# Kernel tuning notes

Hardware: AMD Instinct MI355X
Metric: run time of the kernel (lower is better)

Reference implementation:

```python
import jax, jax.numpy as jnp
import numpy as np

B, N, C, H, W = 4, 64, 256, 64, 64
ROI = 7          # roi_samples
S = 3            # ceil(16px / 7) sample points per ROI cell (boxes fixed at 16px)
HALF = 0.125     # fixed normalized half-size -> 16px boxes on 64-grid -> static S
N_INT = ROI * S  # interpolation grid side length (21)


def setup_inputs() -> dict:
    key = jax.random.key(0)
    k1, k2, k3, k4, k5 = jax.random.split(key, 5)
    img = jax.random.normal(k1, (B, C, H, W), jnp.float32)
    cen = jax.random.uniform(k2, (B, N, 2), jnp.float32, minval=0.2, maxval=0.8)
    # boxes_bn22 = [(x1,y1),(x2,y2)], normalized coords, fixed size so that
    # custom_roi_align's ceil(box_px/roi) == S for every box
    boxes = jnp.stack([cen - HALF, cen + HALF], axis=2)  # (B,N,2,2)
    conv_w = jax.random.normal(k3, (C, C, ROI, ROI), jnp.float32) * 0.02
    conv_b = jnp.zeros((C,), jnp.float32)
    cxcywh_w = jax.random.normal(k4, (C, 4), jnp.float32) * 0.02
    cxcywh_b = jnp.zeros((C,), jnp.float32)
    posenc_w = jax.random.normal(k5, (C, C + 2), jnp.float32) * 0.02
    posenc_b = jnp.zeros((C,), jnp.float32)
    return {"image_tokens_bchw": img, "boxes_bn22": boxes,
            "conv_w": conv_w, "conv_b": conv_b,
            "cxcywh_w": cxcywh_w, "cxcywh_b": cxcywh_b,
            "posenc_w": posenc_w, "posenc_b": posenc_b}


def _pe_1d(coord, num_feats):
    # DETR/SAM-style sinusoidal PE of a scalar coordinate -> (n, num_feats)
    dim_t = 10000.0 ** (2.0 * (jnp.arange(num_feats) // 2) / num_feats)
    pos = coord[:, None] * (2.0 * jnp.pi) / dim_t.astype(coord.dtype)
    enc = jnp.stack([jnp.sin(pos[:, 0::2]), jnp.cos(pos[:, 1::2])], axis=-1)
    return enc.reshape(coord.shape[0], num_feats)


def _roi_align(img_bchw, boxes_f4, bidx):
    # Faithful vectorization of custom_roi_align: per-box uniform sample grid,
    # bilinear grid_sample (align_corners=True, border pad), then SxS avg-pool.
    nsx = W / (W - 1.0)
    nsy = H / (H - 1.0)
    t = jnp.arange(N_INT, dtype=img_bchw.dtype) / (N_INT - 1)

    def one(b, box):
        x1, y1, x2, y2 = box[0] * nsx, box[1] * nsy, box[2] * nsx, box[3] * nsy
        hsx = (x2 - x1) / (2 * N_INT)
        hsy = (y2 - y1) / (2 * N_INT)
        gx = (x1 + hsx) + t * (x2 - x1 - 2 * hsx)  # linspace over box interior
        gy = (y1 + hsy) + t * (y2 - y1 - 2 * hsy)
        # align_corners=True pixel coords; border padding == clamp
        px = jnp.clip(gx * (W - 1), 0.0, W - 1.0)
        py = jnp.clip(gy * (H - 1), 0.0, H - 1.0)
        x0f, y0f = jnp.floor(px), jnp.floor(py)
        wx, wy = px - x0f, py - y0f
        x0 = jnp.clip(x0f.astype(jnp.int32), 0, W - 1)
        x1i = jnp.clip(x0 + 1, 0, W - 1)
        y0 = jnp.clip(y0f.astype(jnp.int32), 0, H - 1)
        y1i = jnp.clip(y0 + 1, 0, H - 1)
        img = img_bchw[b]                               # (C,H,W)
        v00 = img[:, y0[:, None], x0[None, :]]          # (C,N_INT,N_INT)
        v01 = img[:, y0[:, None], x1i[None, :]]
        v10 = img[:, y1i[:, None], x0[None, :]]
        v11 = img[:, y1i[:, None], x1i[None, :]]
        top = v00 + (v01 - v00) * wx[None, None, :]
        bot = v10 + (v11 - v10) * wx[None, None, :]
        samp = top + (bot - top) * wy[None, :, None]    # (C,N_INT,N_INT)
        # avg_pool2d with kernel (S,S) stride (S,S)
        return samp.reshape(C, ROI, S, ROI, S).mean(axis=(2, 4))  # (C,ROI,ROI)

    return jax.vmap(one)(bidx, boxes_f4)


def reference(image_tokens_bchw, boxes_bn22, conv_w, conv_b,
              cxcywh_w, cxcywh_b, posenc_w, posenc_b):
    boxes_f4 = boxes_bn22.reshape(B * N, 4)
    bidx = jnp.repeat(jnp.arange(B), N)
    roi = _roi_align(image_tokens_bchw, boxes_f4, bidx)      # (BN,C,ROI,ROI)
    # 7x7 conv over a 7x7 map -> 1x1: a plain contraction
    img_enc = (jnp.einsum('nchw,ochw->no', roi, conv_w) + conv_b).reshape(B, N, C)

    cen = boxes_bn22.mean(axis=2)                            # (B,N,2) cx,cy
    wh = boxes_bn22[:, :, 1] - boxes_bn22[:, :, 0]           # (B,N,2) w,h
    cxcywh = jnp.concatenate([cen, wh], axis=-1)             # (B,N,4)
    flat = cxcywh.reshape(B * N, 4)
    x_enc = _pe_1d(flat[:, 0], C // 2)
    y_enc = _pe_1d(flat[:, 1], C // 2)
    pe_tok = jnp.concatenate([y_enc, x_enc, flat[:, 3:4], flat[:, 2:3]], axis=-1)
    pos_enc = (pe_tok @ posenc_w.T + posenc_b).reshape(B, N, C)
    base = cxcywh @ cxcywh_w.T + cxcywh_b                    # (B,N,C)
    return base + pos_enc + img_enc
```

## Files before the change

### kernel.cpp

```cpp
#include <hip/hip_runtime.h>

static constexpr int KDIM = 12544;
static constexpr float TWO_PI = 6.28318530717958647692f;

typedef float f32x4 __attribute__((ext_vector_type(4)));
typedef short bf16x8 __attribute__((ext_vector_type(8)));

__device__ inline float bf2f(unsigned short u) {
    union { unsigned int i; float f; } x; x.i = ((unsigned int)u) << 16; return x.f;
}
__device__ inline unsigned short f2bf(float f) {
    union { float f; unsigned int i; } x; x.f = f;
    unsigned int r = (x.i + 0x7FFFu + ((x.i >> 16) & 1u)) >> 16;
    return (unsigned short)r;
}

__global__ __launch_bounds__(256) void k_prep(
    const float* __restrict__ boxes,
    const float* __restrict__ cxw, const float* __restrict__ cxb,
    const float* __restrict__ pw,  const float* __restrict__ pb,
    const float* __restrict__ cb,
    const float* __restrict__ img, const float* __restrict__ convw,
    float* __restrict__ out,
    unsigned short* __restrict__ imgT, unsigned short* __restrict__ Wt,
    float4* __restrict__ lutx, float4* __restrict__ luty)
{
    __shared__ float smem[12544];
    const int bid = blockIdx.x;
    const int tid = threadIdx.x;

    if (bid < 256) {
        const int n = bid;
        const float bx1 = boxes[n*4+0], by1 = boxes[n*4+1];
        const float bx2 = boxes[n*4+2], by2 = boxes[n*4+3];
        const float cx = 0.5f*(bx1+bx2), cy = 0.5f*(by1+by2);
        const float wx = bx2-bx1,        wy = by2-by1;

        float* pe = smem;

        if (tid < 128) {
            const int   k     = tid & 63;
            const float coord = (tid < 64) ? cy : cx;
            const float d   = exp2f((float)k * (13.287712379549449f / 64.0f));
            const float arg = coord * TWO_PI / d;
            float s, c;
            sincosf(arg, &s, &c);
            const int base = (tid < 64) ? 0 : 128;
            pe[base + 2*k]     = s;
            pe[base + 2*k + 1] = c;
        } else if (tid == 128) {
            pe[256] = wy;
            pe[257] = wx;
        } else if (tid >= 160 && tid < 202) {
            const int  t   = tid - 160;
            const bool isx = (t < 21);
            const int  i   = isx ? t : (t - 21);
            const float ns = 64.0f / 63.0f;
            const float a1 = (isx ? bx1 : by1) * ns;
            const float a2 = (isx ? bx2 : by2) * ns;
            const float hs = (a2 - a1) * (1.0f / 42.0f);
            const float tt = (float)i * (1.0f / 20.0f);
            const float g  = a1 + hs + tt * (a2 - a1 - 2.0f*hs);
            float p = g * 63.0f;
            p = fminf(fmaxf(p, 0.0f), 63.0f);
            const float p0 = floorf(p);
            const float w  = p - p0;
            int i0 = (int)p0; i0 = min(i0, 63);
            const int i1 = min(i0 + 1, 63);
            (isx ? lutx : luty)[n*21 + i] = make_float4((float)i0, (float)i1, w, 0.0f);
        }
        __syncthreads();

        const int o = tid;
        float acc = pb[o] + cb[o] + cxb[o];
        acc = fmaf(cxw[o*4+0], cx, acc);
        acc = fmaf(cxw[o*4+1], cy, acc);
        acc = fmaf(cxw[o*4+2], wx, acc);
        acc = fmaf(cxw[o*4+3], wy, acc);
        const float* __restrict__ pwr = pw + o*258;
        for (int k = 0; k < 258; ++k)
            acc = fmaf(pe[k], pwr[k], acc);
        out[n*256 + o] = acc;
    } else if (bid < 1280) {
        float (*t)[65] = (float(*)[65])smem;
        const int idx = bid - 256;
        const int b   = idx >> 8;
        const int rem = idx & 255;
        const int c0  = (rem & 3) * 64;
        const int p0  = (rem >> 2) * 64;
        const int col = tid & 63;
        const int r4  = tid >> 6;
        #pragma unroll
        for (int i = 0; i < 16; ++i) {
            const int row = i*4 + r4;
            t[row][col] = img[((size_t)(b*256 + c0 + row)) * 4096 + p0 + col];
        }
        __syncthreads();
        #pragma unroll
        for (int i = 0; i < 16; ++i) {
            const int prow = i*4 + r4;
            imgT[((size_t)(b*4096 + p0 + prow)) * 256 + c0 + col] = f2bf(t[col][prow]);
        }
    } else {
        const int o = bid - 1280;
        #pragma unroll
        for (int i = 0; i < 49; ++i)
            smem[i*256 + tid] = convw[(size_t)o*12544 + i*256 + tid];
        __syncthreads();
        for (int ij = 0; ij < 49; ++ij)
            Wt[(size_t)o*12544 + ij*256 + tid] = f2bf(smem[tid*49 + ij]);
    }
}

__global__ __launch_bounds__(256) void k_fused(
    const unsigned short* __restrict__ imgT,
    const unsigned short* __restrict__ Wt,
    const float4* __restrict__ lutx, const float4* __restrict__ luty,
    float* __restrict__ partial)
{
    __shared__ __align__(16) char ldsA[16384];
    __shared__ __align__(16) char ldsW[32768];

    const int mt = blockIdx.x;
    const int ij = blockIdx.y;
    const int m0 = mt * 32;
    const int pi = ij / 7, pj = ij - pi * 7;
    const int tid = threadIdx.x;
    const int w = tid >> 6, l = tid & 63;
    const int l15 = l & 15, lg = l >> 4;
    const int c4 = l * 4;

    for (int bi = 0; bi < 8; ++bi) {
        const int r = w * 8 + bi;
        const int n = m0 + r;
        const int b = n >> 6;
        const unsigned short* __restrict__ base = imgT + ((size_t)b << 20) + c4;

        const float4 lx0 = lutx[n*21 + pj*3 + 0];
        const float4 lx1 = lutx[n*21 + pj*3 + 1];
        const float4 lx2 = lutx[n*21 + pj*3 + 2];

        float a0 = 0.f, a1 = 0.f, a2 = 0.f, a3 = 0.f;
        #pragma unroll
        for (int si = 0; si < 3; ++si) {
            const float4 ly = luty[n*21 + pi*3 + si];
            const unsigned short* __restrict__ r0 = base + (((int)ly.x) << 14);
            const unsigned short* __restrict__ r1 = base + (((int)ly.y) << 14);
            const float wyy = ly.z;
            const float4 lxs[3] = {lx0, lx1, lx2};
            #pragma unroll
            for (int sj = 0; sj < 3; ++sj) {
                const float4 lx = lxs[sj];
                const int x0 = ((int)lx.x) << 8, x1 = ((int)lx.y) << 8;
                const float wxx = lx.z;
                const ushort4 v00 = *(const ushort4*)(r0 + x0);
                const ushort4 v01 = *(const ushort4*)(r0 + x1);
                const ushort4 v10 = *(const ushort4*)(r1 + x0);
                const ushort4 v11 = *(const ushort4*)(r1 + x1);
                {
                    const float t = fmaf(bf2f(v01.x) - bf2f(v00.x), wxx, bf2f(v00.x));
                    const float u = fmaf(bf2f(v11.x) - bf2f(v10.x), wxx, bf2f(v10.x));
                    a0 += fmaf(u - t, wyy, t);
                }
                {
                    const float t = fmaf(bf2f(v01.y) - bf2f(v00.y), wxx, bf2f(v00.y));
                    const float u = fmaf(bf2f(v11.y) - bf2f(v10.y), wxx, bf2f(v10.y));
                    a1 += fmaf(u - t, wyy, t);
                }
                {
                    const float t = fmaf(bf2f(v01.z) - bf2f(v00.z), wxx, bf2f(v00.z));
                    const float u = fmaf(bf2f(v11.z) - bf2f(v10.z), wxx, bf2f(v10.z));
                    a2 += fmaf(u - t, wyy, t);
                }
                {
                    const float t = fmaf(bf2f(v01.w) - bf2f(v00.w), wxx, bf2f(v00.w));
                    const float u = fmaf(bf2f(v11.w) - bf2f(v10.w), wxx, bf2f(v10.w));
                    a3 += fmaf(u - t, wyy, t);
                }
            }
        }
        const float s = 1.0f / 9.0f;
        ushort4 o4;
        o4.x = f2bf(a0 * s); o4.y = f2bf(a1 * s);
        o4.z = f2bf(a2 * s); o4.w = f2bf(a3 * s);
        *(ushort4*)&ldsA[(r * 512 + l * 8) ^ ((r & 7) << 4)] = o4;
    }
    __syncthreads();

    float* __restrict__ pp = partial + (size_t)ij * 65536;
    const int bcol = w * 16 + l15;
    #pragma unroll 1
    for (int oc = 0; oc < 4; ++oc) {
        if (oc) __syncthreads();
        #pragma unroll
        for (int it = 0; it < 8; ++it) {
            const int chunk = tid + it * 256;
            const int row = chunk >> 5, ci = chunk & 31;
            *(float4*)&ldsW[(row * 512 + ci * 16) ^ ((row & 7) << 4)] =
                *(const float4*)(Wt + (size_t)(oc * 64 + row) * KDIM + ij * 256 + ci * 8);
        }
        __syncthreads();

        f32x4 acc[2] = {};
        #pragma unroll
        for (int ks = 0; ks < 8; ++ks) {
            const int koff = ks * 64 + lg * 16;
            const bf16x8 bfrag =
                *(const bf16x8*)&ldsW[(bcol * 512 + koff) ^ ((bcol & 7) << 4)];
            #pragma unroll
            for (int mi = 0; mi < 2; ++mi) {
                const int arow = mi * 16 + l15;
                const bf16x8 afrag =
                    *(const bf16x8*)&ldsA[(arow * 512 + koff) ^ ((arow & 7) << 4)];
                acc[mi] = __builtin_amdgcn_mfma_f32_16x16x32_bf16(afrag, bfrag, acc[mi], 0, 0, 0);
            }
        }
        #pragma unroll
        for (int mi = 0; mi < 2; ++mi)
            #pragma unroll
            for (int j = 0; j < 4; ++j)
                pp[(m0 + mi * 16 + lg * 4 + j) * 256 + oc * 64 + bcol] = acc[mi][j];
    }
}

__global__ __launch_bounds__(256) void k_reduce(
    const float* __restrict__ partial, float* __restrict__ out)
{
    const int e = blockIdx.x * 256 + threadIdx.x;
    float s = out[e];
    #pragma unroll
    for (int ij = 0; ij < 49; ++ij)
        s += partial[(size_t)ij * 65536 + e];
    out[e] = s;
}

extern "C" void kernel_launch(void* const* d_in, const int* in_sizes, int n_in,
                              void* d_out, int out_size, void* d_ws, size_t ws_size,
                              hipStream_t stream)
{
    const float* img   = (const float*)d_in[0];
    const float* boxes = (const float*)d_in[1];
    const float* convw = (const float*)d_in[2];
    const float* convb = (const float*)d_in[3];
    const float* cxw   = (const float*)d_in[4];
    const float* cxb   = (const float*)d_in[5];
    const float* pw    = (const float*)d_in[6];
    const float* pb    = (const float*)d_in[7];
    float* out = (float*)d_out;

    unsigned short* imgT    = (unsigned short*)d_ws;
    unsigned short* Wt      = (unsigned short*)((char*)d_ws + 8388608);
    float*          partial = (float*)((char*)d_ws + 14811136);
    float4*         lutx    = (float4*)((char*)d_ws + 27656192);
    float4*         luty    = (float4*)((char*)d_ws + 27742208);

    k_prep<<<1536, 256, 0, stream>>>(boxes, cxw, cxb, pw, pb, convb,
                                     img, convw, out, imgT, Wt, lutx, luty);
    k_fused<<<dim3(8, 49), 256, 0, stream>>>(imgT, Wt, lutx, luty, partial);
    k_reduce<<<256, 256, 0, stream>>>(partial, out);
}
```

Before: 131.9 us.

## Replace split-K partial buffer and reduce kernel with atomic accumulation

The fused kernel now adds its per-cell GEMM results straight into the output with float atomics, so the 49-way partial buffer and the separate reduce kernel are gone. The M tile is halved from 32 to 16 rows, which doubles the grid to 16x49 blocks for more parallelism. This removes one kernel launch and a large write-then-read of partial sums. In exchange, each block reloads the same weight slice for half as many rows, and 49-way atomic contention per output element makes the summation order nondeterministic.

```diff
diff --git a/kernel.cpp b/kernel.cpp
--- a/kernel.cpp
+++ b/kernel.cpp
@@ -116,22 +116,22 @@
     const unsigned short* __restrict__ imgT,
     const unsigned short* __restrict__ Wt,
     const float4* __restrict__ lutx, const float4* __restrict__ luty,
-    float* __restrict__ partial)
+    float* __restrict__ out)
 {
-    __shared__ __align__(16) char ldsA[16384];
+    __shared__ __align__(16) char ldsA[8192];
     __shared__ __align__(16) char ldsW[32768];
 
     const int mt = blockIdx.x;
     const int ij = blockIdx.y;
-    const int m0 = mt * 32;
+    const int m0 = mt * 16;
     const int pi = ij / 7, pj = ij - pi * 7;
     const int tid = threadIdx.x;
     const int w = tid >> 6, l = tid & 63;
     const int l15 = l & 15, lg = l >> 4;
     const int c4 = l * 4;
 
-    for (int bi = 0; bi < 8; ++bi) {
-        const int r = w * 8 + bi;
+    for (int bi = 0; bi < 4; ++bi) {
+        const int r = w * 4 + bi;
         const int n = m0 + r;
         const int b = n >> 6;
         const unsigned short* __restrict__ base = imgT + ((size_t)b << 20) + c4;
@@ -187,7 +187,6 @@
     }
     __syncthreads();
 
-    float* __restrict__ pp = partial + (size_t)ij * 65536;
     const int bcol = w * 16 + l15;
     #pragma unroll 1
     for (int oc = 0; oc < 4; ++oc) {
@@ -201,37 +200,20 @@
         }
         __syncthreads();
 
-        f32x4 acc[2] = {};
+        f32x4 acc = {};
         #pragma unroll
         for (int ks = 0; ks < 8; ++ks) {
             const int koff = ks * 64 + lg * 16;
             const bf16x8 bfrag =
                 *(const bf16x8*)&ldsW[(bcol * 512 + koff) ^ ((bcol & 7) << 4)];
-            #pragma unroll
-            for (int mi = 0; mi < 2; ++mi) {
-                const int arow = mi * 16 + l15;
-                const bf16x8 afrag =
-                    *(const bf16x8*)&ldsA[(arow * 512 + koff) ^ ((arow & 7) << 4)];
-                acc[mi] = __builtin_amdgcn_mfma_f32_16x16x32_bf16(afrag, bfrag, acc[mi], 0, 0, 0);
-            }
-        }
-        #pragma unroll
-        for (int mi = 0; mi < 2; ++mi)
-            #pragma unroll
-            for (int j = 0; j < 4; ++j)
-                pp[(m0 + mi * 16 + lg * 4 + j) * 256 + oc * 64 + bcol] = acc[mi][j];
+            const bf16x8 afrag =
+                *(const bf16x8*)&ldsA[(l15 * 512 + koff) ^ ((l15 & 7) << 4)];
+            acc = __builtin_amdgcn_mfma_f32_16x16x32_bf16(afrag, bfrag, acc, 0, 0, 0);
+        }
+        #pragma unroll
+        for (int j = 0; j < 4; ++j)
+            unsafeAtomicAdd(&out[(m0 + lg * 4 + j) * 256 + oc * 64 + bcol], acc[j]);
     }
-}
-
-__global__ __launch_bounds__(256) void k_reduce(
-    const float* __restrict__ partial, float* __restrict__ out)
-{
-    const int e = blockIdx.x * 256 + threadIdx.x;
-    float s = out[e];
-    #pragma unroll
-    for (int ij = 0; ij < 49; ++ij)
-        s += partial[(size_t)ij * 65536 + e];
-    out[e] = s;
 }
 
 extern "C" void kernel_launch(void* const* d_in, const int* in_sizes, int n_in,
@@ -248,14 +230,12 @@
     const float* pb    = (const float*)d_in[7];
     float* out = (float*)d_out;
 
-    unsigned short* imgT    = (unsigned short*)d_ws;
-    unsigned short* Wt      = (unsigned short*)((char*)d_ws + 8388608);
-    float*          partial = (float*)((char*)d_ws + 14811136);
-    float4*         lutx    = (float4*)((char*)d_ws + 27656192);
-    float4*         luty    = (float4*)((char*)d_ws + 27742208);
+    unsigned short* imgT = (unsigned short*)d_ws;
+    unsigned short* Wt   = (unsigned short*)((char*)d_ws + 8388608);
+    float4*         lutx = (float4*)((char*)d_ws + 14811136);
+    float4*         luty = (float4*)((char*)d_ws + 14897152);
 
     k_prep<<<1536, 256, 0, stream>>>(boxes, cxw, cxb, pw, pb, convb,
                                      img, convw, out, imgT, Wt, lutx, luty);
-    k_fused<<<dim3(8, 49), 256, 0, stream>>>(imgT, Wt, lutx, luty, partial);
-    k_reduce<<<256, 256, 0, stream>>>(partial, out);
-}
+    k_fused<<<dim3(16, 49), 256, 0, stream>>>(imgT, Wt, lutx, luty, out);
+}
```

After: 128.4 us, median of 2. 2.7% less time.
